# Kernel tuning notes

Measured on AMD Instinct MI355X. Metric: run time of the kernel, lower is better.

## Reference

```python
import jax, jax.numpy as jnp
import numpy as np

B, T, C, H, L, NC = 4096, 400, 42, 16, 2, 2  # batch, seq_len, input_size, hidden, layers, classes


def setup_inputs() -> dict:
    key = jax.random.key(0)
    ks = jax.random.split(key, 12)
    k = 1.0 / np.sqrt(H)  # torch nn.RNN uniform(-1/sqrt(H), 1/sqrt(H)) init scale
    u = lambda kk, shape: jax.random.uniform(kk, shape, jnp.float32, -k, k)
    return {
        "x": jax.random.normal(ks[0], (B, C * T), jnp.float32),
        "h0": jnp.zeros((L, B, H), jnp.float32),
        "W_ih0": u(ks[1], (H, C)),
        "W_hh0": u(ks[2], (H, H)),
        "b_ih0": u(ks[3], (H,)),
        "b_hh0": u(ks[4], (H,)),
        "W_ih1": u(ks[5], (H, H)),
        "W_hh1": u(ks[6], (H, H)),
        "b_ih1": u(ks[7], (H,)),
        "b_hh1": u(ks[8], (H,)),
        "W_fc": jax.random.normal(ks[9], (NC, H), jnp.float32) * np.sqrt(2.0 / H),  # kaiming_normal_
        "b_fc": u(ks[10], (NC,)),
    }


def _rnn_layer(seq, h, W_ih, W_hh, b_ih, b_hh):
    # seq: (B, T, F); vanilla tanh RNN, batch_first. Returns full output sequence (B, T, H).
    bias = b_ih + b_hh

    def step(h, xt):  # xt: (B, F), h: (B, H)
        h = jnp.tanh(xt @ W_ih.T + h @ W_hh.T + bias)
        return h, h

    _, ys = jax.lax.scan(step, h, seq.transpose(1, 0, 2))  # ys: (T, B, H)
    return ys.transpose(1, 0, 2)


def reference(x, h0, W_ih0, W_hh0, b_ih0, b_hh0, W_ih1, W_hh1, b_ih1, b_hh1, W_fc, b_fc):
    # x.view(B, -1, 400).transpose(2, 1) -> (B, T=400, C=42)
    xs = x.reshape(B, C, T).transpose(0, 2, 1)
    y0 = _rnn_layer(xs, h0[0], W_ih0, W_hh0, b_ih0, b_hh0)  # (B, T, H)
    y1 = _rnn_layer(y0, h0[1], W_ih1, W_hh1, b_ih1, b_hh1)  # (B, T, H)
    h_t = y1[:, -1, :]  # last timestep of top layer
    return h_t @ W_fc.T + b_fc  # (B, NC)
```

## Files before the change

### kernel.cpp

```cpp
#include <hip/hip_runtime.h>

#define NB 4096
#define NT 400
#define NCH 42
#define NH 16
#define NT4 100

#define RORI(v,K) __builtin_amdgcn_update_dpp(0, (v), 0x120+(K), 0xF, 0xF, true)
#define RORF(v,K) __int_as_float(__builtin_amdgcn_update_dpp(0, __float_as_int(v), 0x120+(K), 0xF, 0xF, true))

static __device__ __forceinline__ float fast_tanh(float x) {
  float ax = __builtin_fabsf(x);
  float e  = __expf(2.0f * ax);
  float r  = __builtin_fmaf(-2.0f, __builtin_amdgcn_rcpf(e + 1.0f), 1.0f);
  return __builtin_copysignf(r, x);
}

__global__ __launch_bounds__(128) void proj0_kernel(
    const float* __restrict__ x, const float* __restrict__ Wih0,
    const float* __restrict__ bih0, const float* __restrict__ bhh0,
    float4* __restrict__ P)
{
  __shared__ float Wl[NH * NCH];
  __shared__ float bl[NH];
  const int tid = threadIdx.x;
  for (int i = tid; i < NH * NCH; i += 128) Wl[i] = Wih0[i];
  if (tid < NH) bl[tid] = bih0[tid] + bhh0[tid];
  __syncthreads();

  const int b  = blockIdx.x;
  const int t4 = tid;
  if (t4 >= NT4) return;

  float4 acc[NH];
#pragma unroll
  for (int j = 0; j < NH; ++j) { float bb = bl[j]; acc[j] = make_float4(bb, bb, bb, bb); }

  const float* xrow = x + (size_t)b * (NCH * NT) + t4 * 4;
  for (int c = 0; c < NCH; ++c) {
    float4 xv = *(const float4*)(xrow + (size_t)c * NT);
#pragma unroll
    for (int j = 0; j < NH; ++j) {
      float w = Wl[j * NCH + c];
      acc[j].x = __builtin_fmaf(xv.x, w, acc[j].x);
      acc[j].y = __builtin_fmaf(xv.y, w, acc[j].y);
      acc[j].z = __builtin_fmaf(xv.z, w, acc[j].z);
      acc[j].w = __builtin_fmaf(xv.w, w, acc[j].w);
    }
  }
  float4* Pout = P + ((size_t)t4 * NB + b) * NH;
#pragma unroll
  for (int j = 0; j < NH; ++j) Pout[j] = acc[j];
}

__global__ __launch_bounds__(256) void rnn_seq_kernel(
    const float4* __restrict__ P, const float* __restrict__ h0in,
    const float* __restrict__ Whh0, const float* __restrict__ Wih1,
    const float* __restrict__ Whh1, const float* __restrict__ bih1,
    const float* __restrict__ bhh1, const float* __restrict__ Wfc,
    const float* __restrict__ bfc, float* __restrict__ out)
{
  const int gtid = blockIdx.x * blockDim.x + threadIdx.x;
  const int b = gtid >> 4;
  const int j = threadIdx.x & 15;

  float w0[NH], wi1[NH], wh1[NH];
  w0[0]  = Whh0[j * NH + j];
  wi1[0] = Wih1[j * NH + j];
  wh1[0] = Whh1[j * NH + j];
#define LOADW(K) { int sj = RORI(j, K) & 15; \
  w0[K]  = Whh0[j * NH + sj]; \
  wi1[K] = Wih1[j * NH + sj]; \
  wh1[K] = Whh1[j * NH + sj]; }
  LOADW(1) LOADW(2) LOADW(3) LOADW(4) LOADW(5) LOADW(6) LOADW(7) LOADW(8)
  LOADW(9) LOADW(10) LOADW(11) LOADW(12) LOADW(13) LOADW(14) LOADW(15)
#undef LOADW
  const float b1   = bih1[j] + bhh1[j];
  const float wfc0 = Wfc[j];
  const float wfc1 = Wfc[NH + j];

  float h0 = h0in[b * NH + j];
  float h1 = h0in[(size_t)NB * NH + b * NH + j];

  const size_t pstride = (size_t)NB * NH;
  const size_t pidx    = (size_t)b * NH + j;
  float4 pc = P[pidx];

  for (int t4 = 0; t4 < NT4; ++t4) {
    const int nx = (t4 + 1 < NT4) ? (t4 + 1) : (NT4 - 1);
    float4 pn = P[pidx + (size_t)nx * pstride];
    float pv[4] = {pc.x, pc.y, pc.z, pc.w};
#pragma unroll
    for (int q = 0; q < 4; ++q) {
      float a  = __builtin_fmaf(h0, w0[0], pv[q]);
      float a2 = 0.0f;
#define L0T(K) { float hv = RORF(h0, K); \
  if ((K) & 1) a2 = __builtin_fmaf(hv, w0[K], a2); \
  else         a  = __builtin_fmaf(hv, w0[K], a); }
      L0T(1) L0T(2) L0T(3) L0T(4) L0T(5) L0T(6) L0T(7) L0T(8)
      L0T(9) L0T(10) L0T(11) L0T(12) L0T(13) L0T(14) L0T(15)
#undef L0T
      float h0n = fast_tanh(a + a2);

      float c1 = __builtin_fmaf(h0n, wi1[0], b1);
      float c2 = h1 * wh1[0];
#define L1A(K) { float hv = RORF(h0n, K); \
  if ((K) & 1) c2 = __builtin_fmaf(hv, wi1[K], c2); \
  else         c1 = __builtin_fmaf(hv, wi1[K], c1); }
      L1A(1) L1A(2) L1A(3) L1A(4) L1A(5) L1A(6) L1A(7) L1A(8)
      L1A(9) L1A(10) L1A(11) L1A(12) L1A(13) L1A(14) L1A(15)
#undef L1A
#define L1B(K) { float hv = RORF(h1, K); \
  if ((K) & 1) c1 = __builtin_fmaf(hv, wh1[K], c1); \
  else         c2 = __builtin_fmaf(hv, wh1[K], c2); }
      L1B(1) L1B(2) L1B(3) L1B(4) L1B(5) L1B(6) L1B(7) L1B(8)
      L1B(9) L1B(10) L1B(11) L1B(12) L1B(13) L1B(14) L1B(15)
#undef L1B
      h1 = fast_tanh(c1 + c2);
      h0 = h0n;
    }
    pc = pn;
  }

  float v0 = h1 * wfc0;
  float v1 = h1 * wfc1;
#pragma unroll
  for (int m = 8; m >= 1; m >>= 1) {
    v0 += __shfl_xor(v0, m, 16);
    v1 += __shfl_xor(v1, m, 16);
  }
  if (j == 0) {
    float* o = out + (size_t)b * 2;
    o[0] = v0 + bfc[0];
    o[1] = v1 + bfc[1];
  }
}

extern "C" void kernel_launch(void* const* d_in, const int* in_sizes, int n_in,
                              void* d_out, int out_size, void* d_ws, size_t ws_size,
                              hipStream_t stream) {
  const float* x    = (const float*)d_in[0];
  const float* h0   = (const float*)d_in[1];
  const float* Wih0 = (const float*)d_in[2];
  const float* Whh0 = (const float*)d_in[3];
  const float* bih0 = (const float*)d_in[4];
  const float* bhh0 = (const float*)d_in[5];
  const float* Wih1 = (const float*)d_in[6];
  const float* Whh1 = (const float*)d_in[7];
  const float* bih1 = (const float*)d_in[8];
  const float* bhh1 = (const float*)d_in[9];
  const float* Wfc  = (const float*)d_in[10];
  const float* bfc  = (const float*)d_in[11];
  float* outp = (float*)d_out;
  float4* P = (float4*)d_ws;

  proj0_kernel<<<NB, 128, 0, stream>>>(x, Wih0, bih0, bhh0, P);
  rnn_seq_kernel<<<(NB * NH) / 256, 256, 0, stream>>>(
      P, h0, Whh0, Wih1, Whh1, bih1, bhh1, Wfc, bfc, outp);
}
```

Before: 523.9 us.

## Store layer-0 input projection in fp16 and deepen prefetch in recurrence

The intermediate input-projection buffer P is now written as packed half precision instead of fp32, which halves the workspace traffic between the projection kernel and the recurrent kernel. The recurrent kernel prefetches two time-blocks ahead instead of one to hide load latency. The projection kernel's channel loop is also unrolled by 7 so more x loads are in flight at once. Rounding the pre-activations to fp16 adds error that passes through 400 recurrent steps, so the final outputs may drift from the fp32 reference.

```diff
diff --git a/kernel.cpp b/kernel.cpp
--- a/kernel.cpp
+++ b/kernel.cpp
@@ -1,4 +1,5 @@
 #include <hip/hip_runtime.h>
+#include <hip/hip_fp16.h>
 
 #define NB 4096
 #define NT 400
@@ -16,10 +17,15 @@
   return __builtin_copysignf(r, x);
 }
 
+static __device__ __forceinline__ uint pack_h2(float a, float b) {
+  __half ha = __float2half(a), hb = __float2half(b);
+  return (uint)__half_as_ushort(ha) | ((uint)__half_as_ushort(hb) << 16);
+}
+
 __global__ __launch_bounds__(128) void proj0_kernel(
     const float* __restrict__ x, const float* __restrict__ Wih0,
     const float* __restrict__ bih0, const float* __restrict__ bhh0,
-    float4* __restrict__ P)
+    uint4* __restrict__ P)
 {
   __shared__ float Wl[NH * NCH];
   __shared__ float bl[NH];
@@ -37,24 +43,39 @@
   for (int j = 0; j < NH; ++j) { float bb = bl[j]; acc[j] = make_float4(bb, bb, bb, bb); }
 
   const float* xrow = x + (size_t)b * (NCH * NT) + t4 * 4;
-  for (int c = 0; c < NCH; ++c) {
-    float4 xv = *(const float4*)(xrow + (size_t)c * NT);
 #pragma unroll
-    for (int j = 0; j < NH; ++j) {
-      float w = Wl[j * NCH + c];
-      acc[j].x = __builtin_fmaf(xv.x, w, acc[j].x);
-      acc[j].y = __builtin_fmaf(xv.y, w, acc[j].y);
-      acc[j].z = __builtin_fmaf(xv.z, w, acc[j].z);
-      acc[j].w = __builtin_fmaf(xv.w, w, acc[j].w);
+  for (int cc = 0; cc < NCH; cc += 7) {
+    float4 xv[7];
+#pragma unroll
+    for (int u = 0; u < 7; ++u) xv[u] = *(const float4*)(xrow + (size_t)(cc + u) * NT);
+#pragma unroll
+    for (int u = 0; u < 7; ++u) {
+#pragma unroll
+      for (int j = 0; j < NH; ++j) {
+        float w = Wl[j * NCH + cc + u];
+        acc[j].x = __builtin_fmaf(xv[u].x, w, acc[j].x);
+        acc[j].y = __builtin_fmaf(xv[u].y, w, acc[j].y);
+        acc[j].z = __builtin_fmaf(xv[u].z, w, acc[j].z);
+        acc[j].w = __builtin_fmaf(xv[u].w, w, acc[j].w);
+      }
     }
   }
-  float4* Pout = P + ((size_t)t4 * NB + b) * NH;
+
+  uint4* Pout = P + ((size_t)t4 * NB + b) * 8;
 #pragma unroll
-  for (int j = 0; j < NH; ++j) Pout[j] = acc[j];
+  for (int jp = 0; jp < 8; ++jp) {
+    const float4 a0 = acc[2 * jp], a1 = acc[2 * jp + 1];
+    uint4 ov;
+    ov.x = pack_h2(a0.x, a0.y);
+    ov.y = pack_h2(a0.z, a0.w);
+    ov.z = pack_h2(a1.x, a1.y);
+    ov.w = pack_h2(a1.z, a1.w);
+    Pout[jp] = ov;
+  }
 }
 
 __global__ __launch_bounds__(256) void rnn_seq_kernel(
-    const float4* __restrict__ P, const float* __restrict__ h0in,
+    const uint2* __restrict__ P, const float* __restrict__ h0in,
     const float* __restrict__ Whh0, const float* __restrict__ Wih1,
     const float* __restrict__ Whh1, const float* __restrict__ bih1,
     const float* __restrict__ bhh1, const float* __restrict__ Wfc,
@@ -84,12 +105,18 @@
 
   const size_t pstride = (size_t)NB * NH;
   const size_t pidx    = (size_t)b * NH + j;
-  float4 pc = P[pidx];
+  uint2 pc = P[pidx];
+  uint2 pn = P[pidx + pstride];
 
   for (int t4 = 0; t4 < NT4; ++t4) {
-    const int nx = (t4 + 1 < NT4) ? (t4 + 1) : (NT4 - 1);
-    float4 pn = P[pidx + (size_t)nx * pstride];
-    float pv[4] = {pc.x, pc.y, pc.z, pc.w};
+    const int nx = (t4 + 2 < NT4) ? (t4 + 2) : (NT4 - 1);
+    uint2 p2 = P[pidx + (size_t)nx * pstride];
+
+    union { uint2 u; __half2 h[2]; } cv; cv.u = pc;
+    float2 f0 = __half22float2(cv.h[0]);
+    float2 f1 = __half22float2(cv.h[1]);
+    float pv[4] = {f0.x, f0.y, f1.x, f1.y};
+
 #pragma unroll
     for (int q = 0; q < 4; ++q) {
       float a  = __builtin_fmaf(h0, w0[0], pv[q]);
@@ -120,6 +147,7 @@
       h0 = h0n;
     }
     pc = pn;
+    pn = p2;
   }
 
   float v0 = h1 * wfc0;
@@ -152,9 +180,8 @@
   const float* Wfc  = (const float*)d_in[10];
   const float* bfc  = (const float*)d_in[11];
   float* outp = (float*)d_out;
-  float4* P = (float4*)d_ws;
 
-  proj0_kernel<<<NB, 128, 0, stream>>>(x, Wih0, bih0, bhh0, P);
+  proj0_kernel<<<NB, 128, 0, stream>>>(x, Wih0, bih0, bhh0, (uint4*)d_ws);
   rnn_seq_kernel<<<(NB * NH) / 256, 256, 0, stream>>>(
-      P, h0, Whh0, Wih1, Whh1, bih1, bhh1, Wfc, bfc, outp);
+      (const uint2*)d_ws, h0, Whh0, Wih1, Whh1, bih1, bhh1, Wfc, bfc, outp);
 }
```

After: 550.8 us. 1.05x slower.
